# Kernel optimization log

Measured on AMD Instinct MI355X. Metric: run time of the kernel, lower is better.

## Reference

```python
import jax, jax.numpy as jnp
import numpy as np

B, N, D, H = 256, 128, 2048, 16
DH = D // H  # 128 == N, required by the module's broadcast coefs*out


def setup_inputs() -> dict:
    key = jax.random.key(0)
    k0, k1, k2, k3, k4, k5 = jax.random.split(key, 6)
    batchinput = jax.random.normal(k0, (B, N, D), dtype=jnp.float32)
    # Conv1d(D, DH, 1, bias=False) == pointwise linear D -> DH
    Wa = jax.random.normal(k1, (D, DH), dtype=jnp.float32) * 0.02
    # Conv1d(DH, 1, 1) with bias
    Wb = jax.random.normal(k2, (DH, 1), dtype=jnp.float32) * 0.02
    bb = jax.random.normal(k3, (1,), dtype=jnp.float32) * 0.02
    Wc = jax.random.normal(k4, (DH, 1), dtype=jnp.float32) * 0.02
    bc = jax.random.normal(k5, (1,), dtype=jnp.float32) * 0.02
    bias = jnp.full((DH,), 0.01, dtype=jnp.float32)
    return {"batchinput": batchinput, "Wa": Wa, "Wb": Wb, "bb": bb,
            "Wc": Wc, "bc": bc, "bias": bias}


def reference(batchinput, Wa, Wb, bb, Wc, bc, bias):
    # All n_head heads share weights and dropout=0 -> identical; mean over heads
    # equals a single head. n_steps=1 (multi-step is shape-incompatible for H>1).
    h = jnp.einsum("bnd,de->bne", batchinput, Wa)          # [B,N,DH]
    t1 = h @ Wb + bb                                        # [B,N,1]
    t2 = h @ Wc + bc                                        # [B,N,1]
    # torch: temp1.permute -> [B,N,1]; temp2 stays [B,1,N]; broadcast add
    scores = t1 + jnp.swapaxes(t2, 1, 2)                    # [B,N,N]
    # F.softmax with dim=None on a 3D tensor -> dim=1
    coefs = jax.nn.softmax(jax.nn.leaky_relu(scores, negative_slope=0.2), axis=1)
    re = coefs * h + bias                                   # [B,N,N]*[B,N,DH], DH==N
    re = re + h                                             # residual=True
    return re
```

## Files before the change

### kernel.cpp

```cpp
#include <hip/hip_runtime.h>
#include <hip/hip_bf16.h>
#include <stdint.h>

typedef short bf16x8 __attribute__((ext_vector_type(8)));
typedef float f32x4  __attribute__((ext_vector_type(4)));

#define Nn 128
#define Dd 2048
#define DH 128
#define BK 64
#define HP 130

__device__ __forceinline__ unsigned short f2bf(float f) {
  unsigned int u = __float_as_uint(f);
  u = (u + 0x7fffu + ((u >> 16) & 1u)) >> 16;
  return (unsigned short)u;
}
__device__ __forceinline__ float bf2f(unsigned short s) { return __uint_as_float(((unsigned int)s) << 16); }
__device__ __forceinline__ float bflo(unsigned int p) { return __uint_as_float(p << 16); }
__device__ __forceinline__ float bfhi(unsigned int p) { return __uint_as_float(p & 0xffff0000u); }

__device__ __forceinline__ int detect_f32(const unsigned int* __restrict__ X) {
  int cnt = 0;
#pragma unroll
  for (int i = 0; i < 64; ++i) {
    unsigned int e = (X[i] >> 23) & 0xffu;
    cnt += (e < 200u) ? 1 : 0;
  }
  return cnt >= 32;
}

__global__ __launch_bounds__(256) void transpose_wa(const void* __restrict__ Wa,
                                                    short* __restrict__ WaT,
                                                    const unsigned int* __restrict__ X) {
  __shared__ int flg;
  __shared__ short tile[32][33];
  if (threadIdx.x == 0) flg = detect_f32(X);
  __syncthreads();
  const int f32 = flg;
  const int tx = threadIdx.x & 31, ty = threadIdx.x >> 5;
  const int d0 = blockIdx.x * 32, e0 = blockIdx.y * 32;
#pragma unroll
  for (int r = 0; r < 4; ++r) {
    const int src = (d0 + ty + 8 * r) * DH + e0 + tx;
    short v;
    if (f32) v = (short)f2bf(((const float*)Wa)[src]);
    else     v = ((const short*)Wa)[src];
    tile[ty + 8 * r][tx] = v;
  }
  __syncthreads();
#pragma unroll
  for (int r = 0; r < 4; ++r)
    WaT[(e0 + ty + 8 * r) * Dd + d0 + tx] = tile[tx][ty + 8 * r];
}

union SMemU {
  struct { short A[2][128 * BK]; short Bm[2][128 * BK]; } st;
  unsigned short h[128 * HP];
};

template <bool F32>
__device__ __forceinline__ void gat_body(
    const void* __restrict__ Xv, const short* __restrict__ WaT,
    const void* __restrict__ Wb, const void* __restrict__ bbp,
    const void* __restrict__ Wc, const void* __restrict__ bcp,
    const void* __restrict__ biasp, void* __restrict__ outv)
{
  __shared__ SMemU sm;
  __shared__ float t1s[128], t2s[128], wbs[128], wcs[128], biass[128];
  __shared__ float red[512];
  __shared__ float mrec[128], srec[128];
  __shared__ int flg;

  const int tid = threadIdx.x;
  if (tid == 0) flg = detect_f32((const unsigned int*)Xv);
  __syncthreads();
  if ((flg != 0) != F32) return;

  const int b   = blockIdx.x;
  const int l   = tid & 63;
  const int w   = tid >> 6;
  const int wr  = w >> 2;
  const int wc4 = w & 3;

  if (tid < 128) {
    wbs[tid]   = F32 ? ((const float*)Wb)[tid]    : bf2f(((const unsigned short*)Wb)[tid]);
    wcs[tid]   = F32 ? ((const float*)Wc)[tid]    : bf2f(((const unsigned short*)Wc)[tid]);
    biass[tid] = F32 ? ((const float*)biasp)[tid] : bf2f(((const unsigned short*)biasp)[tid]);
  }

  f32x4 acc[4][2];
#pragma unroll
  for (int i = 0; i < 4; ++i)
#pragma unroll
    for (int j = 0; j < 2; ++j) acc[i][j] = (f32x4){0.f, 0.f, 0.f, 0.f};

  const int rowh = tid >> 3;
  const int g    = tid & 7;
  const size_t xbase = (size_t)b * Nn * Dd;

  float4 pa4[2][2];
  bf16x8 paB[2];
  bf16x8 pb[2];

  auto load_g = [&](int k0) {
#pragma unroll
    for (int c = 0; c < 2; ++c) {
      const int row = c * 64 + rowh;
      const int off = row * Dd + k0 + g * 8;
      if (F32) {
        const float* p = (const float*)Xv + xbase + off;
        pa4[c][0] = *(const float4*)p;
        pa4[c][1] = *(const float4*)(p + 4);
      } else {
        paB[c] = *(const bf16x8*)((const short*)Xv + xbase + off);
      }
      pb[c] = *(const bf16x8*)(WaT + off);
    }
  };

  auto store_lds = [&](int p) {
#pragma unroll
    for (int c = 0; c < 2; ++c) {
      const int row  = c * 64 + rowh;
      const int phys = row * 64 + ((g ^ (row & 7)) << 3);
      bf16x8 av;
      if (F32) {
        av[0] = (short)f2bf(pa4[c][0].x); av[1] = (short)f2bf(pa4[c][0].y);
        av[2] = (short)f2bf(pa4[c][0].z); av[3] = (short)f2bf(pa4[c][0].w);
        av[4] = (short)f2bf(pa4[c][1].x); av[5] = (short)f2bf(pa4[c][1].y);
        av[6] = (short)f2bf(pa4[c][1].z); av[7] = (short)f2bf(pa4[c][1].w);
      } else {
        av = paB[c];
      }
      *(bf16x8*)&sm.st.A[p][phys]  = av;
      *(bf16x8*)&sm.st.Bm[p][phys] = pb[c];
    }
  };

  auto mfma_step = [&](int p) {
#pragma unroll
    for (int ks = 0; ks < 2; ++ks) {
      const int gb = ks * 4 + (l >> 4);
      bf16x8 aF[4], bF[2];
#pragma unroll
      for (int mr = 0; mr < 4; ++mr) {
        const int row = wr * 64 + mr * 16 + (l & 15);
        aF[mr] = *(const bf16x8*)&sm.st.A[p][row * 64 + ((gb ^ (row & 7)) << 3)];
      }
#pragma unroll
      for (int nc = 0; nc < 2; ++nc) {
        const int row = wc4 * 32 + nc * 16 + (l & 15);
        bF[nc] = *(const bf16x8*)&sm.st.Bm[p][row * 64 + ((gb ^ (row & 7)) << 3)];
      }
#pragma unroll
      for (int mr = 0; mr < 4; ++mr)
#pragma unroll
        for (int nc = 0; nc < 2; ++nc)
          acc[mr][nc] = __builtin_amdgcn_mfma_f32_16x16x32_bf16(aF[mr], bF[nc], acc[mr][nc], 0, 0, 0);
    }
  };

  load_g(0);
  store_lds(0);
  load_g(BK);
  __syncthreads();
  int p = 0;
  for (int k0 = 0; k0 < Dd; k0 += BK) {
    mfma_step(p);
    if (k0 + BK < Dd) {
      store_lds(p ^ 1);
      if (k0 + 2 * BK < Dd) load_g(k0 + 2 * BK);
    }
    __syncthreads();
    p ^= 1;
  }

#pragma unroll
  for (int mr = 0; mr < 4; ++mr) {
    const int row0 = wr * 64 + mr * 16 + (l >> 4) * 4;
#pragma unroll
    for (int nc = 0; nc < 2; ++nc) {
      const int col = wc4 * 32 + nc * 16 + (l & 15);
#pragma unroll
      for (int r = 0; r < 4; ++r)
        sm.h[(row0 + r) * HP + col] = f2bf(acc[mr][nc][r]);
    }
  }
  __syncthreads();

  {
    const int i    = (tid >> 1) & 127;
    const int half = tid & 1;
    const float* wv = ((tid < 256) ? wbs : wcs) + half * 64;
    const unsigned int* hr = (const unsigned int*)&sm.h[i * HP] + half * 32;
    float a0 = 0.f, a1 = 0.f;
#pragma unroll 8
    for (int e2 = 0; e2 < 32; ++e2) {
      const unsigned int pr = hr[e2];
      a0 += bflo(pr) * wv[2 * e2];
      a1 += bfhi(pr) * wv[2 * e2 + 1];
    }
    red[tid] = a0 + a1;
  }
  __syncthreads();
  if (tid < 256) {
    const int j = tid & 127;
    const int sel = tid >> 7;
    const void* bsel = sel ? bcp : bbp;
    const float bv = F32 ? ((const float*)bsel)[0] : bf2f(((const unsigned short*)bsel)[0]);
    const float t = red[sel * 256 + 2 * j] + red[sel * 256 + 2 * j + 1] + bv;
    if (sel == 0) t1s[j] = t; else t2s[j] = t;
  }
  __syncthreads();

  {
    const int j  = tid & 127;
    const int hf = tid >> 7;
    const float t2j = t2s[j];
    float mloc = -1e30f;
#pragma unroll 8
    for (int ii = 0; ii < 32; ++ii) {
      float s = t1s[hf * 32 + ii] + t2j;
      s = (s > 0.f) ? s : 0.2f * s;
      mloc = fmaxf(mloc, s);
    }
    red[hf * 128 + j] = mloc;
    __syncthreads();
    const float mj = fmaxf(fmaxf(red[j], red[128 + j]), fmaxf(red[256 + j], red[384 + j]));
    float sl = 0.f;
#pragma unroll 8
    for (int ii = 0; ii < 32; ++ii) {
      float s = t1s[hf * 32 + ii] + t2j;
      s = (s > 0.f) ? s : 0.2f * s;
      sl += __expf(s - mj);
    }
    __syncthreads();
    red[hf * 128 + j] = sl;
    __syncthreads();
    if (hf == 0) {
      mrec[j] = mj;
      srec[j] = 1.f / (red[j] + red[128 + j] + red[256 + j] + red[384 + j]);
    }
  }
  __syncthreads();

  {
    const int jp = (tid & 63) * 2;
    const int rq = tid >> 6;
    const float m0 = mrec[jp],     s0 = srec[jp];
    const float m1 = mrec[jp + 1], s1 = srec[jp + 1];
    const float u0 = t2s[jp], u1 = t2s[jp + 1];
    const float b0 = biass[jp], b1 = biass[jp + 1];
#pragma unroll 4
    for (int ii = 0; ii < 16; ++ii) {
      const int i = ii * 8 + rq;
      const float t1i = t1s[i];
      float sA = t1i + u0; sA = (sA > 0.f) ? sA : 0.2f * sA;
      float sB = t1i + u1; sB = (sB > 0.f) ? sB : 0.2f * sB;
      const float pA = __expf(sA - m0) * s0;
      const float pB = __expf(sB - m1) * s1;
      const unsigned int pr = *(const unsigned int*)&sm.h[i * HP + jp];
      const float oA = bflo(pr) * (1.f + pA) + b0;
      const float oB = bfhi(pr) * (1.f + pB) + b1;
      if (F32) {
        float2 v2; v2.x = oA; v2.y = oB;
        *(float2*)((float*)outv + (size_t)b * Nn * DH + i * DH + jp) = v2;
      } else {
        const unsigned int pk = (unsigned int)f2bf(oA) | ((unsigned int)f2bf(oB) << 16);
        *(unsigned int*)((unsigned short*)outv + (size_t)b * Nn * DH + i * DH + jp) = pk;
      }
    }
  }
}

__global__ __launch_bounds__(512, 2) void fused_gat_f32(
    const void* __restrict__ X, const short* __restrict__ WaT,
    const void* __restrict__ Wb, const void* __restrict__ bb,
    const void* __restrict__ Wc, const void* __restrict__ bc,
    const void* __restrict__ bias, void* __restrict__ out) {
  gat_body<true>(X, WaT, Wb, bb, Wc, bc, bias, out);
}

__global__ __launch_bounds__(512, 2) void fused_gat_bf16(
    const void* __restrict__ X, const short* __restrict__ WaT,
    const void* __restrict__ Wb, const void* __restrict__ bb,
    const void* __restrict__ Wc, const void* __restrict__ bc,
    const void* __restrict__ bias, void* __restrict__ out) {
  gat_body<false>(X, WaT, Wb, bb, Wc, bc, bias, out);
}

extern "C" void kernel_launch(void* const* d_in, const int* in_sizes, int n_in,
                              void* d_out, int out_size, void* d_ws, size_t ws_size,
                              hipStream_t stream) {
  const void* X    = d_in[0];
  const void* Wa   = d_in[1];
  const void* Wb   = d_in[2];
  const void* bb   = d_in[3];
  const void* Wc   = d_in[4];
  const void* bc   = d_in[5];
  const void* bias = d_in[6];
  short* WaT = (short*)d_ws;

  transpose_wa<<<dim3(64, 4), 256, 0, stream>>>(Wa, WaT, (const unsigned int*)X);
  fused_gat_f32 <<<256, 512, 0, stream>>>(X, WaT, Wb, bb, Wc, bc, bias, d_out);
  fused_gat_bf16<<<256, 512, 0, stream>>>(X, WaT, Wb, bb, Wc, bc, bias, d_out);
}
```

Measured before the change: 403.8 us.

## Load GEMM fragments directly from global memory and merge dtype kernels via flag

Drops the LDS double-buffered staging of X and WaT tiles. Each wave now loads its MFMA A and B fragments straight from global memory, converting fp32 to bf16 in registers. The dtype detection result is written to a workspace flag by the transpose kernel, so one fused kernel launch replaces the two per-dtype launches. This removes LDS traffic and barriers from the main loop and frees shared memory. The cost is redundant global reads of X across the four column waves and of WaT across the two row waves, with no explicit prefetch to hide latency.

```diff
diff --git a/kernel.cpp b/kernel.cpp
--- a/kernel.cpp
+++ b/kernel.cpp
@@ -8,7 +8,6 @@
 #define Nn 128
 #define Dd 2048
 #define DH 128
-#define BK 64
 #define HP 130
 
 __device__ __forceinline__ unsigned short f2bf(float f) {
@@ -32,12 +31,14 @@
 
 __global__ __launch_bounds__(256) void transpose_wa(const void* __restrict__ Wa,
                                                     short* __restrict__ WaT,
-                                                    const unsigned int* __restrict__ X) {
+                                                    const unsigned int* __restrict__ X,
+                                                    int* __restrict__ flag) {
   __shared__ int flg;
   __shared__ short tile[32][33];
   if (threadIdx.x == 0) flg = detect_f32(X);
   __syncthreads();
   const int f32 = flg;
+  if (blockIdx.x == 0 && blockIdx.y == 0 && threadIdx.x == 0) *flag = f32;
   const int tx = threadIdx.x & 31, ty = threadIdx.x >> 5;
   const int d0 = blockIdx.x * 32, e0 = blockIdx.y * 32;
 #pragma unroll
@@ -54,34 +55,23 @@
     WaT[(e0 + ty + 8 * r) * Dd + d0 + tx] = tile[tx][ty + 8 * r];
 }
 
-union SMemU {
-  struct { short A[2][128 * BK]; short Bm[2][128 * BK]; } st;
-  unsigned short h[128 * HP];
-};
-
 template <bool F32>
 __device__ __forceinline__ void gat_body(
     const void* __restrict__ Xv, const short* __restrict__ WaT,
     const void* __restrict__ Wb, const void* __restrict__ bbp,
     const void* __restrict__ Wc, const void* __restrict__ bcp,
-    const void* __restrict__ biasp, void* __restrict__ outv)
+    const void* __restrict__ biasp, void* __restrict__ outv,
+    unsigned short* __restrict__ h, float* t1s, float* t2s,
+    float* wbs, float* wcs, float* biass, float* red, float* mrec, float* srec)
 {
-  __shared__ SMemU sm;
-  __shared__ float t1s[128], t2s[128], wbs[128], wcs[128], biass[128];
-  __shared__ float red[512];
-  __shared__ float mrec[128], srec[128];
-  __shared__ int flg;
-
   const int tid = threadIdx.x;
-  if (tid == 0) flg = detect_f32((const unsigned int*)Xv);
-  __syncthreads();
-  if ((flg != 0) != F32) return;
-
   const int b   = blockIdx.x;
   const int l   = tid & 63;
   const int w   = tid >> 6;
   const int wr  = w >> 2;
   const int wc4 = w & 3;
+  const int fr  = l & 15;
+  const int fq  = l >> 4;
 
   if (tid < 128) {
     wbs[tid]   = F32 ? ((const float*)Wb)[tid]    : bf2f(((const unsigned short*)Wb)[tid]);
@@ -95,63 +85,36 @@
 #pragma unroll
     for (int j = 0; j < 2; ++j) acc[i][j] = (f32x4){0.f, 0.f, 0.f, 0.f};
 
-  const int rowh = tid >> 3;
-  const int g    = tid & 7;
   const size_t xbase = (size_t)b * Nn * Dd;
-
-  float4 pa4[2][2];
-  bf16x8 paB[2];
-  bf16x8 pb[2];
-
-  auto load_g = [&](int k0) {
-#pragma unroll
-    for (int c = 0; c < 2; ++c) {
-      const int row = c * 64 + rowh;
-      const int off = row * Dd + k0 + g * 8;
-      if (F32) {
-        const float* p = (const float*)Xv + xbase + off;
-        pa4[c][0] = *(const float4*)p;
-        pa4[c][1] = *(const float4*)(p + 4);
-      } else {
-        paB[c] = *(const bf16x8*)((const short*)Xv + xbase + off);
+  const float* Xf = (const float*)Xv + xbase;
+  const short* Xs = (const short*)Xv + xbase;
+
+  for (int k0 = 0; k0 < Dd; k0 += 64) {
+#pragma unroll
+    for (int ks = 0; ks < 2; ++ks) {
+      const int kk = k0 + ks * 32 + fq * 8;
+      bf16x8 aF[4], bF[2];
+#pragma unroll
+      for (int mr = 0; mr < 4; ++mr) {
+        const int row = wr * 64 + mr * 16 + fr;
+        if (F32) {
+          const float* p = Xf + (size_t)row * Dd + kk;
+          float4 u0 = *(const float4*)p;
+          float4 u1 = *(const float4*)(p + 4);
+          bf16x8 t;
+          t[0] = (short)f2bf(u0.x); t[1] = (short)f2bf(u0.y);
+          t[2] = (short)f2bf(u0.z); t[3] = (short)f2bf(u0.w);
+          t[4] = (short)f2bf(u1.x); t[5] = (short)f2bf(u1.y);
+          t[6] = (short)f2bf(u1.z); t[7] = (short)f2bf(u1.w);
+          aF[mr] = t;
+        } else {
+          aF[mr] = *(const bf16x8*)(Xs + (size_t)row * Dd + kk);
+        }
       }
-      pb[c] = *(const bf16x8*)(WaT + off);
-    }
-  };
-
-  auto store_lds = [&](int p) {
-#pragma unroll
-    for (int c = 0; c < 2; ++c) {
-      const int row  = c * 64 + rowh;
-      const int phys = row * 64 + ((g ^ (row & 7)) << 3);
-      bf16x8 av;
-      if (F32) {
-        av[0] = (short)f2bf(pa4[c][0].x); av[1] = (short)f2bf(pa4[c][0].y);
-        av[2] = (short)f2bf(pa4[c][0].z); av[3] = (short)f2bf(pa4[c][0].w);
-        av[4] = (short)f2bf(pa4[c][1].x); av[5] = (short)f2bf(pa4[c][1].y);
-        av[6] = (short)f2bf(pa4[c][1].z); av[7] = (short)f2bf(pa4[c][1].w);
-      } else {
-        av = paB[c];
-      }
-      *(bf16x8*)&sm.st.A[p][phys]  = av;
-      *(bf16x8*)&sm.st.Bm[p][phys] = pb[c];
-    }
-  };
-
-  auto mfma_step = [&](int p) {
-#pragma unroll
-    for (int ks = 0; ks < 2; ++ks) {
-      const int gb = ks * 4 + (l >> 4);
-      bf16x8 aF[4], bF[2];
-#pragma unroll
-      for (int mr = 0; mr < 4; ++mr) {
-        const int row = wr * 64 + mr * 16 + (l & 15);
-        aF[mr] = *(const bf16x8*)&sm.st.A[p][row * 64 + ((gb ^ (row & 7)) << 3)];
-      }
 #pragma unroll
       for (int nc = 0; nc < 2; ++nc) {
-        const int row = wc4 * 32 + nc * 16 + (l & 15);
-        bF[nc] = *(const bf16x8*)&sm.st.Bm[p][row * 64 + ((gb ^ (row & 7)) << 3)];
+        const int col = wc4 * 32 + nc * 16 + fr;
+        bF[nc] = *(const bf16x8*)(WaT + (size_t)col * Dd + kk);
       }
 #pragma unroll
       for (int mr = 0; mr < 4; ++mr)
@@ -159,32 +122,17 @@
         for (int nc = 0; nc < 2; ++nc)
           acc[mr][nc] = __builtin_amdgcn_mfma_f32_16x16x32_bf16(aF[mr], bF[nc], acc[mr][nc], 0, 0, 0);
     }
-  };
-
-  load_g(0);
-  store_lds(0);
-  load_g(BK);
-  __syncthreads();
-  int p = 0;
-  for (int k0 = 0; k0 < Dd; k0 += BK) {
-    mfma_step(p);
-    if (k0 + BK < Dd) {
-      store_lds(p ^ 1);
-      if (k0 + 2 * BK < Dd) load_g(k0 + 2 * BK);
-    }
-    __syncthreads();
-    p ^= 1;
   }
 
 #pragma unroll
   for (int mr = 0; mr < 4; ++mr) {
-    const int row0 = wr * 64 + mr * 16 + (l >> 4) * 4;
+    const int row0 = wr * 64 + mr * 16 + fq * 4;
 #pragma unroll
     for (int nc = 0; nc < 2; ++nc) {
-      const int col = wc4 * 32 + nc * 16 + (l & 15);
+      const int col = wc4 * 32 + nc * 16 + fr;
 #pragma unroll
       for (int r = 0; r < 4; ++r)
-        sm.h[(row0 + r) * HP + col] = f2bf(acc[mr][nc][r]);
+        h[(row0 + r) * HP + col] = f2bf(acc[mr][nc][r]);
     }
   }
   __syncthreads();
@@ -193,7 +141,7 @@
     const int i    = (tid >> 1) & 127;
     const int half = tid & 1;
     const float* wv = ((tid < 256) ? wbs : wcs) + half * 64;
-    const unsigned int* hr = (const unsigned int*)&sm.h[i * HP] + half * 32;
+    const unsigned int* hr = (const unsigned int*)&h[i * HP] + half * 32;
     float a0 = 0.f, a1 = 0.f;
 #pragma unroll 8
     for (int e2 = 0; e2 < 32; ++e2) {
@@ -260,7 +208,7 @@
       float sB = t1i + u1; sB = (sB > 0.f) ? sB : 0.2f * sB;
       const float pA = __expf(sA - m0) * s0;
       const float pB = __expf(sB - m1) * s1;
-      const unsigned int pr = *(const unsigned int*)&sm.h[i * HP + jp];
+      const unsigned int pr = *(const unsigned int*)&h[i * HP + jp];
       const float oA = bflo(pr) * (1.f + pA) + b0;
       const float oB = bfhi(pr) * (1.f + pB) + b1;
       if (F32) {
@@ -274,20 +222,20 @@
   }
 }
 
-__global__ __launch_bounds__(512, 2) void fused_gat_f32(
+__global__ __launch_bounds__(512, 2) void fused_gat(
     const void* __restrict__ X, const short* __restrict__ WaT,
     const void* __restrict__ Wb, const void* __restrict__ bb,
     const void* __restrict__ Wc, const void* __restrict__ bc,
-    const void* __restrict__ bias, void* __restrict__ out) {
-  gat_body<true>(X, WaT, Wb, bb, Wc, bc, bias, out);
-}
-
-__global__ __launch_bounds__(512, 2) void fused_gat_bf16(
-    const void* __restrict__ X, const short* __restrict__ WaT,
-    const void* __restrict__ Wb, const void* __restrict__ bb,
-    const void* __restrict__ Wc, const void* __restrict__ bc,
-    const void* __restrict__ bias, void* __restrict__ out) {
-  gat_body<false>(X, WaT, Wb, bb, Wc, bc, bias, out);
+    const void* __restrict__ bias, void* __restrict__ out,
+    const int* __restrict__ flag)
+{
+  __shared__ unsigned short h[128 * HP];
+  __shared__ float t1s[128], t2s[128], wbs[128], wcs[128], biass[128];
+  __shared__ float red[512], mrec[128], srec[128];
+  if (*flag)
+    gat_body<true >(X, WaT, Wb, bb, Wc, bc, bias, out, h, t1s, t2s, wbs, wcs, biass, red, mrec, srec);
+  else
+    gat_body<false>(X, WaT, Wb, bb, Wc, bc, bias, out, h, t1s, t2s, wbs, wcs, biass, red, mrec, srec);
 }
 
 extern "C" void kernel_launch(void* const* d_in, const int* in_sizes, int n_in,
@@ -301,8 +249,8 @@
   const void* bc   = d_in[5];
   const void* bias = d_in[6];
   short* WaT = (short*)d_ws;
-
-  transpose_wa<<<dim3(64, 4), 256, 0, stream>>>(Wa, WaT, (const unsigned int*)X);
-  fused_gat_f32 <<<256, 512, 0, stream>>>(X, WaT, Wb, bb, Wc, bc, bias, d_out);
-  fused_gat_bf16<<<256, 512, 0, stream>>>(X, WaT, Wb, bb, Wc, bc, bias, d_out);
-}
+  int*   flag = (int*)((char*)d_ws + (512 << 10));
+
+  transpose_wa<<<dim3(64, 4), 256, 0, stream>>>(Wa, WaT, (const unsigned int*)X, flag);
+  fused_gat<<<256, 512, 0, stream>>>(X, WaT, Wb, bb, Wc, bc, bias, d_out, flag);
+}
```

New measurement: 482.9 us. 1.2x slower.
